# Kernel tuning notes

Measured on AMD Instinct MI355X. Metric: run time of the kernel, lower is better.

## Reference

```python
import jax, jax.numpy as jnp
import numpy as np

STRIDE = 8
OUT = 96                 # feature map size fh = fw
SEARCH = OUT * STRIDE    # 768, search image size
RATIOS = [0.33, 0.5, 1.0, 2.0, 3.0]
SCALES = [4, 8, 16]
PRE_NMS = 1024
POST_NMS = 256
NMS_THRESH = 0.7


def _make_anchors():
    # anchor widths/heights per (ratio, scale), base size = stride * scale
    ws, hs = [], []
    for r in RATIOS:
        for s in SCALES:
            ws.append(STRIDE * s / np.sqrt(r))
            hs.append(STRIDE * s * np.sqrt(r))
    ws = np.asarray(ws, np.float32)  # [A]
    hs = np.asarray(hs, np.float32)
    ori = SEARCH // 2 - (OUT // 2) * STRIDE
    c = ori + STRIDE * np.arange(OUT, dtype=np.float32)
    cy, cx = np.meshgrid(c, c, indexing="ij")  # [OUT, OUT]
    x1 = cx[None] - ws[:, None, None] * 0.5  # [A, OUT, OUT]
    y1 = cy[None] - hs[:, None, None] * 0.5
    x2 = cx[None] + ws[:, None, None] * 0.5
    y2 = cy[None] + hs[:, None, None] * 0.5
    return np.stack([x1, y1, x2, y2], axis=-1).reshape(-1, 4)  # [A*K, 4]


def setup_inputs() -> dict:
    key = jax.random.key(0)
    k1, k2 = jax.random.split(key)
    pred_cls = jax.random.normal(k1, (32, 30, 96, 96), jnp.float32)
    pred_reg = jax.random.normal(k2, (32, 60, 96, 96), jnp.float32) * 0.2
    anchors = jnp.asarray(_make_anchors())
    return {"pred_cls": pred_cls, "pred_reg": pred_reg, "anchors": anchors}


def _nms_pad(boxes, scores):
    """boxes [N,4] sorted by score desc, scores [N]. Returns [POST_NMS,5] padded."""
    x1, y1, x2, y2 = boxes[:, 0], boxes[:, 1], boxes[:, 2], boxes[:, 3]
    areas = (x2 - x1 + 1.0) * (y2 - y1 + 1.0)
    ix1 = jnp.maximum(x1[:, None], x1[None, :])
    iy1 = jnp.maximum(y1[:, None], y1[None, :])
    ix2 = jnp.minimum(x2[:, None], x2[None, :])
    iy2 = jnp.minimum(y2[:, None], y2[None, :])
    inter = jnp.maximum(ix2 - ix1 + 1.0, 0.0) * jnp.maximum(iy2 - iy1 + 1.0, 0.0)
    iou = inter / (areas[:, None] + areas[None, :] - inter)
    n = boxes.shape[0]
    idxs = jnp.arange(n)

    def body(keep, i):
        sup = keep[i] & (iou[i] > NMS_THRESH) & (idxs > i)
        return keep & ~sup, None

    keep, _ = jax.lax.scan(body, jnp.ones((n,), bool), idxs)
    pos = jnp.cumsum(keep) - 1
    dst = jnp.where(keep & (pos < POST_NMS), pos, POST_NMS)  # pad row for dropped
    rows = jnp.concatenate([scores[:, None], boxes], axis=1)  # [N,5] score first
    out = jnp.zeros((POST_NMS + 1, 5), boxes.dtype).at[dst].set(rows)
    return out[:POST_NMS]


def reference(pred_cls, pred_reg, anchors):
    b, a2, h, w = pred_cls.shape
    A = a2 // 2
    # log-softmax over the 2-way fg/bg channel; take foreground log-probs
    logp = jax.nn.log_softmax(pred_cls.reshape(b, 2, A, h, w), axis=1)
    scores = logp[:, 1].reshape(b, -1)  # [b, A*h*w]
    # deltas: (b,4A,h,w) -> (b,4,A,h,w) -> (b,A,h,w,4) -> (b,A*h*w,4)
    deltas = pred_reg.reshape(b, 4, A, h, w).transpose(0, 2, 3, 4, 1).reshape(b, -1, 4)
    aw = anchors[:, 2] - anchors[:, 0] + 1.0
    ah = anchors[:, 3] - anchors[:, 1] + 1.0
    acx = anchors[:, 0] + 0.5 * aw
    acy = anchors[:, 1] + 0.5 * ah
    dx, dy, dw, dh = deltas[..., 0], deltas[..., 1], deltas[..., 2], deltas[..., 3]
    pcx = dx * aw + acx
    pcy = dy * ah + acy
    pw = jnp.exp(dw) * aw
    ph = jnp.exp(dh) * ah
    boxes = jnp.stack([pcx - 0.5 * pw, pcy - 0.5 * ph, pcx + 0.5 * pw, pcy + 0.5 * ph], axis=-1)
    boxes = jnp.clip(boxes, 0.0, SEARCH - 1.0)  # clip to image
    top_s, top_i = jax.lax.top_k(scores, PRE_NMS)  # per-image pre-NMS top-k
    top_b = jnp.take_along_axis(boxes, top_i[..., None], axis=1)  # [b,PRE,4]
    return jax.vmap(_nms_pad)(top_b, top_s)  # [b, POST_NMS, 5]
```

## Files before the change

### kernel.cpp

```cpp
#include <hip/hip_runtime.h>
#include <stdint.h>

#define NANCH 138240
#define NANCH4 34560
#define B_CNT 32
#define PRE 1024
#define POST 256
#define BINS 8192
#define CAP 4096
#define SBLK 15
#define SLICE4 2304
#define TLOC 192
#define LOCCAP 273
#define PAD_KEY 0xFFFFFFFFFFFFFFFFull

typedef unsigned long long u64;

__device__ __forceinline__ unsigned key32(float sc) {
    unsigned u = __float_as_uint(sc);
    unsigned s = (u & 0x80000000u) ? ~u : (u | 0x80000000u);
    return ~s;
}

__device__ __forceinline__ unsigned key_of(float x0, float x1) {
    float m  = fmaxf(x0, x1);
    float e0 = expf(x0 - m);
    float e1 = expf(x1 - m);
    float sc = (x1 - m) - logf(e0 + e1);
    return key32(sc);
}

__device__ __forceinline__ void decode_box(const float* __restrict__ reg,
                                           const float* __restrict__ anch,
                                           int b, int idx, float box[4]) {
    const float* rb = reg + (size_t)b * 4 * NANCH;
    float dx = rb[idx];
    float dy = rb[idx + NANCH];
    float dw = rb[idx + 2 * NANCH];
    float dh = rb[idx + 3 * NANCH];
    float ax1 = anch[idx * 4 + 0], ay1 = anch[idx * 4 + 1];
    float ax2 = anch[idx * 4 + 2], ay2 = anch[idx * 4 + 3];
    float aw  = __fadd_rn(__fsub_rn(ax2, ax1), 1.0f);
    float ah  = __fadd_rn(__fsub_rn(ay2, ay1), 1.0f);
    float acx = __fadd_rn(ax1, __fmul_rn(0.5f, aw));
    float acy = __fadd_rn(ay1, __fmul_rn(0.5f, ah));
    float pcx = __fadd_rn(__fmul_rn(dx, aw), acx);
    float pcy = __fadd_rn(__fmul_rn(dy, ah), acy);
    float pw  = __fmul_rn(expf(dw), aw);
    float ph  = __fmul_rn(expf(dh), ah);
    float hx  = __fmul_rn(0.5f, pw);
    float hy  = __fmul_rn(0.5f, ph);
    box[0] = fminf(fmaxf(__fsub_rn(pcx, hx), 0.0f), 767.0f);
    box[1] = fminf(fmaxf(__fsub_rn(pcy, hy), 0.0f), 767.0f);
    box[2] = fminf(fmaxf(__fadd_rn(pcx, hx), 0.0f), 767.0f);
    box[3] = fminf(fmaxf(__fadd_rn(pcy, hy), 0.0f), 767.0f);
}

__global__ __launch_bounds__(1024) void select_kernel(const float* __restrict__ cls,
                                                      u64* __restrict__ cand) {
    __shared__ unsigned h[BINS];
    __shared__ unsigned s_wsum[16];
    __shared__ u64 loc[LOCCAP];
    __shared__ int s_b;
    __shared__ int lcnt;
    const int b = blockIdx.y;
    const int s = blockIdx.x;
    const int t = threadIdx.x;
    const int lane = t & 63, wid = t >> 6;
    if (t == 0) lcnt = 0;
    for (int i = t; i < BINS; i += 1024) h[i] = 0;
    __syncthreads();

    const float4* cb4 = (const float4*)(cls + (size_t)b * 2 * NANCH);
    const int base4 = s * SLICE4;

    for (int k = 0; k < 3; ++k) {
        int off = k * 1024 + t;
        if (off < SLICE4) {
            int g4 = base4 + off;
            float4 a0 = cb4[g4];
            float4 a1 = cb4[g4 + NANCH4];
            atomicAdd(&h[key_of(a0.x, a1.x) >> 19], 1u);
            atomicAdd(&h[key_of(a0.y, a1.y) >> 19], 1u);
            atomicAdd(&h[key_of(a0.z, a1.z) >> 19], 1u);
            atomicAdd(&h[key_of(a0.w, a1.w) >> 19], 1u);
        }
    }
    __syncthreads();

    unsigned bin[8];
    unsigned seg = 0;
    #pragma unroll
    for (int i = 0; i < 8; ++i) { bin[i] = h[t * 8 + i]; seg += bin[i]; }
    unsigned sc = seg;
    #pragma unroll
    for (int o = 1; o < 64; o <<= 1) {
        unsigned v = (unsigned)__shfl_up((int)sc, o);
        if (lane >= o) sc += v;
    }
    if (lane == 63) s_wsum[wid] = sc;
    __syncthreads();
    unsigned woff = 0;
    for (int i = 0; i < wid; ++i) woff += s_wsum[i];
    unsigned incl = sc + woff;
    unsigned excl = incl - seg;
    if (incl >= TLOC && excl < TLOC) {
        unsigned cum = excl;
        int bs = t * 8 + 7;
        for (int i = 0; i < 8; ++i) {
            if (cum + bin[i] >= TLOC) { bs = t * 8 + i; break; }
            cum += bin[i];
        }
        s_b = bs;
    }
    __syncthreads();
    const int bs = s_b;

    for (int k = 0; k < 3; ++k) {
        int off = k * 1024 + t;
        if (off < SLICE4) {
            int g4 = base4 + off;
            float4 a0 = cb4[g4];
            float4 a1 = cb4[g4 + NANCH4];
            float x0[4] = {a0.x, a0.y, a0.z, a0.w};
            float x1[4] = {a1.x, a1.y, a1.z, a1.w};
            #pragma unroll
            for (int j = 0; j < 4; ++j) {
                unsigned key = key_of(x0[j], x1[j]);
                if ((int)(key >> 19) <= bs) {
                    int pos = atomicAdd(&lcnt, 1);
                    if (pos < LOCCAP)
                        loc[pos] = ((u64)key << 32) | (unsigned)(g4 * 4 + j);
                }
            }
        }
    }
    __syncthreads();
    int n = lcnt; if (n > LOCCAP) n = LOCCAP;
    u64* segp = cand + (size_t)b * CAP + s * LOCCAP;
    for (int i = t; i < LOCCAP; i += 1024)
        segp[i] = (i < n) ? loc[i] : PAD_KEY;
    if (s == 0 && t == 0) cand[(size_t)b * CAP + (CAP - 1)] = PAD_KEY;
}

__global__ __launch_bounds__(512) void lsort_kernel(u64* __restrict__ cand) {
    __shared__ u64 sb[1024];
    const int c = blockIdx.x;
    const int b = blockIdx.y;
    const int t = threadIdx.x;
    u64* seg = cand + (size_t)b * CAP + c * 1024;
    for (int i = t; i < 1024; i += 512) sb[i] = seg[i];
    __syncthreads();
    for (int k = 2; k <= 1024; k <<= 1) {
        for (int j = k >> 1; j > 0; j >>= 1) {
            int i  = ((t & ~(j - 1)) << 1) | (t & (j - 1));
            int p  = i | j;
            bool up = ((i & k) == 0);
            u64 a = sb[i], bb = sb[p];
            if ((a > bb) == up) { sb[i] = bb; sb[p] = a; }
            __syncthreads();
        }
    }
    for (int i = t; i < 1024; i += 512) seg[i] = sb[i];
}

__global__ __launch_bounds__(1024) void merge_kernel(const u64* __restrict__ cand,
                                                     const float* __restrict__ reg,
                                                     const float* __restrict__ anch,
                                                     float* __restrict__ topS,
                                                     float* __restrict__ topB) {
    __shared__ u64 runs[CAP];
    const int r = blockIdx.x;
    const int b = blockIdx.y;
    const int t = threadIdx.x;
    for (int i = t; i < CAP; i += 1024) runs[i] = cand[(size_t)b * CAP + i];
    __syncthreads();

    u64 x = runs[r * 1024 + t];
    int rank = t;
    #pragma unroll
    for (int q = 0; q < 4; ++q) {
        if (q == r) continue;
        const u64* run = &runs[q * 1024];
        int lo = 0, hi = 1024;
        while (lo < hi) {
            int mid = (lo + hi) >> 1;
            if (run[mid] < x) lo = mid + 1; else hi = mid;
        }
        rank += lo;
    }
    if (rank < PRE) {
        int idx = (int)(x & 0xFFFFFFFFu);
        unsigned ks = (unsigned)(x >> 32);
        unsigned s  = ~ks;
        unsigned u  = (s & 0x80000000u) ? (s & 0x7FFFFFFFu) : ~s;
        float scv = __uint_as_float(u);
        float box[4];
        decode_box(reg, anch, b, idx, box);
        topS[b * PRE + rank] = scv;
        float* tb = topB + ((size_t)b * PRE + rank) * 4;
        tb[0] = box[0]; tb[1] = box[1]; tb[2] = box[2]; tb[3] = box[3];
    }
}

__global__ __launch_bounds__(1024) void mask_kernel(const float* __restrict__ topB,
                                                    u64* __restrict__ masks) {
    const int w = blockIdx.x;
    const int b = blockIdx.y;
    const int i = threadIdx.x;
    __shared__ float sx1[64], sy1[64], sx2[64], sy2[64], sar[64];
    if (i < 64) {
        const float* p = topB + ((size_t)b * PRE + w * 64 + i) * 4;
        float x1 = p[0], y1 = p[1], x2 = p[2], y2 = p[3];
        sx1[i] = x1; sy1[i] = y1; sx2[i] = x2; sy2[i] = y2;
        sar[i] = __fmul_rn(__fadd_rn(__fsub_rn(x2, x1), 1.0f),
                           __fadd_rn(__fsub_rn(y2, y1), 1.0f));
    }
    __syncthreads();
    const int jbase = w * 64;
    u64* dst = &masks[((size_t)b * PRE + i) * 16 + w];
    if (i >= jbase + 63) { *dst = 0ull; return; }
    const float* p = topB + ((size_t)b * PRE + i) * 4;
    float x1 = p[0], y1 = p[1], x2 = p[2], y2 = p[3];
    float ar = __fmul_rn(__fadd_rn(__fsub_rn(x2, x1), 1.0f),
                         __fadd_rn(__fsub_rn(y2, y1), 1.0f));
    u64 m = 0ull;
    for (int j = 0; j < 64; j++) {
        int jj = jbase + j;
        if (jj > i) {
            float ix1 = fmaxf(x1, sx1[j]);
            float iy1 = fmaxf(y1, sy1[j]);
            float ix2 = fminf(x2, sx2[j]);
            float iy2 = fminf(y2, sy2[j]);
            float iw = fmaxf(__fadd_rn(__fsub_rn(ix2, ix1), 1.0f), 0.0f);
            float ih = fmaxf(__fadd_rn(__fsub_rn(iy2, iy1), 1.0f), 0.0f);
            float inter = __fmul_rn(iw, ih);
            float denom = __fsub_rn(__fadd_rn(ar, sar[j]), inter);
            float iou = __fdiv_rn(inter, denom);
            if (iou > 0.7f) m |= (1ull << j);
        }
    }
    *dst = m;
}

__device__ __forceinline__ u64 shfl_xor_u64(u64 v, int lanemask) {
    int lo = __shfl_xor((int)(v & 0xFFFFFFFFull), lanemask);
    int hi = __shfl_xor((int)(v >> 32), lanemask);
    return ((u64)(unsigned)hi << 32) | (unsigned)lo;
}

__global__ __launch_bounds__(64) void nms_kernel(const u64* __restrict__ masks,
                                                 const float* __restrict__ topS,
                                                 const float* __restrict__ topB,
                                                 float* __restrict__ out) {
    const int b = blockIdx.x;
    const int t = threadIdx.x;
    __shared__ u64 rem[16];
    __shared__ int kept[POST];
    __shared__ int s_nk;
    if (t < 16) rem[t] = 0ull;
    __syncthreads();

    const u64* mb = masks + (size_t)b * PRE * 16;
    const int w = t >> 2, g = t & 3;
    int prefix = 0;

    u64 dv_cur = mb[(size_t)t * 16 + 0];
    u64 cw_cur[16];
    #pragma unroll
    for (int k = 0; k < 16; ++k)
        cw_cur[k] = mb[((size_t)(g * 16 + k)) * 16 + w];

    for (int c = 0; c < 16; ++c) {
        u64 dv_nxt = 0ull;
        u64 cw_nxt[16];
        if (c < 15) {
            const u64* nb = mb + (size_t)(c + 1) * 64 * 16;
            dv_nxt = nb[(size_t)t * 16 + (c + 1)];
            #pragma unroll
            for (int k = 0; k < 16; ++k)
                cw_nxt[k] = nb[((size_t)(g * 16 + k)) * 16 + w];
        } else {
            #pragma unroll
            for (int k = 0; k < 16; ++k) cw_nxt[k] = 0ull;
        }

        u64 alive = ~rem[c];
        int dlo = (int)(dv_cur & 0xFFFFFFFFull);
        int dhi = (int)(dv_cur >> 32);

        for (int l = 0; l < 64; ++l) {
            unsigned lo = (unsigned)__builtin_amdgcn_readlane(dlo, l);
            unsigned hi = (unsigned)__builtin_amdgcn_readlane(dhi, l);
            u64 dl = ((u64)hi << 32) | lo;
            u64 a = (alive >> l) & 1ull;
            alive &= ~(a ? dl : 0ull);
        }

        if ((alive >> t) & 1ull) {
            int pos = prefix + (int)__popcll(alive & ((1ull << t) - 1ull));
            if (pos < POST) kept[pos] = c * 64 + t;
        }
        prefix += (int)__popcll(alive);

        u64 acc = 0ull;
        #pragma unroll
        for (int k = 0; k < 16; ++k)
            if ((alive >> (g * 16 + k)) & 1ull) acc |= cw_cur[k];
        acc |= shfl_xor_u64(acc, 1);
        acc |= shfl_xor_u64(acc, 2);
        __syncthreads();
        if (g == 0 && w > c) rem[w] |= acc;
        __syncthreads();

        if (prefix >= POST) break;

        dv_cur = dv_nxt;
        #pragma unroll
        for (int k = 0; k < 16; ++k) cw_cur[k] = cw_nxt[k];
    }

    if (t == 0) s_nk = (prefix < POST) ? prefix : POST;
    __syncthreads();
    const int n = s_nk;

    float* ob = out + (size_t)b * POST * 5;
    for (int r = t; r < POST; r += 64) {
        if (r < n) {
            int i = kept[r];
            ob[r * 5 + 0] = topS[b * PRE + i];
            const float* tb = topB + ((size_t)b * PRE + i) * 4;
            ob[r * 5 + 1] = tb[0];
            ob[r * 5 + 2] = tb[1];
            ob[r * 5 + 3] = tb[2];
            ob[r * 5 + 4] = tb[3];
        } else {
            ob[r * 5 + 0] = 0.0f; ob[r * 5 + 1] = 0.0f; ob[r * 5 + 2] = 0.0f;
            ob[r * 5 + 3] = 0.0f; ob[r * 5 + 4] = 0.0f;
        }
    }
}

extern "C" void kernel_launch(void* const* d_in, const int* in_sizes, int n_in,
                              void* d_out, int out_size, void* d_ws, size_t ws_size,
                              hipStream_t stream) {
    const float* cls  = (const float*)d_in[0];
    const float* reg  = (const float*)d_in[1];
    const float* anch = (const float*)d_in[2];

    char* ws = (char*)d_ws;
    float* topS  = (float*)ws;
    float* topB  = (float*)(ws + 131072);
    u64*   cand  = (u64*)(ws + 655360);
    u64*   masks = (u64*)(ws + 1703936);

    select_kernel<<<dim3(SBLK, B_CNT), 1024, 0, stream>>>(cls, cand);
    lsort_kernel <<<dim3(4, B_CNT), 512, 0, stream>>>(cand);
    merge_kernel <<<dim3(4, B_CNT), 1024, 0, stream>>>(cand, reg, anch, topS, topB);
    mask_kernel  <<<dim3(16, B_CNT), 1024, 0, stream>>>(topB, masks);
    nms_kernel   <<<B_CNT, 64, 0, stream>>>(masks, topS, topB, (float*)d_out);
}
```

Measured before the change: 85.13 us.

## Sort candidates inside select kernel and merge 15 runs directly

Each select block now sorts its own candidate list in shared memory with a 512-element bitonic sort, which removes the separate lsort kernel launch. The merge kernel then ranks each candidate by binary-searching all 15 sorted runs of 273 entries instead of 4 runs of 1024. The scores computed in the histogram pass are also kept in registers, so the second pass no longer reloads cls from global memory or recomputes the log-softmax. The trade-offs are more binary searches per candidate, extra shared memory and barriers in select, and higher register pressure.

```diff
diff --git a/kernel.cpp b/kernel.cpp
--- a/kernel.cpp
+++ b/kernel.cpp
@@ -12,6 +12,7 @@
 #define SLICE4 2304
 #define TLOC 192
 #define LOCCAP 273
+#define SORTN 512
 #define PAD_KEY 0xFFFFFFFFFFFFFFFFull
 
 typedef unsigned long long u64;
@@ -59,8 +60,8 @@
 __global__ __launch_bounds__(1024) void select_kernel(const float* __restrict__ cls,
                                                       u64* __restrict__ cand) {
     __shared__ unsigned h[BINS];
+    __shared__ u64 sortbuf[SORTN];
     __shared__ unsigned s_wsum[16];
-    __shared__ u64 loc[LOCCAP];
     __shared__ int s_b;
     __shared__ int lcnt;
     const int b = blockIdx.y;
@@ -69,21 +70,28 @@
     const int lane = t & 63, wid = t >> 6;
     if (t == 0) lcnt = 0;
     for (int i = t; i < BINS; i += 1024) h[i] = 0;
+    if (t < SORTN) sortbuf[t] = PAD_KEY;
     __syncthreads();
 
     const float4* cb4 = (const float4*)(cls + (size_t)b * 2 * NANCH);
     const int base4 = s * SLICE4;
 
+    unsigned kk[3][4];
+    #pragma unroll
     for (int k = 0; k < 3; ++k) {
         int off = k * 1024 + t;
         if (off < SLICE4) {
             int g4 = base4 + off;
             float4 a0 = cb4[g4];
             float4 a1 = cb4[g4 + NANCH4];
-            atomicAdd(&h[key_of(a0.x, a1.x) >> 19], 1u);
-            atomicAdd(&h[key_of(a0.y, a1.y) >> 19], 1u);
-            atomicAdd(&h[key_of(a0.z, a1.z) >> 19], 1u);
-            atomicAdd(&h[key_of(a0.w, a1.w) >> 19], 1u);
+            kk[k][0] = key_of(a0.x, a1.x);
+            kk[k][1] = key_of(a0.y, a1.y);
+            kk[k][2] = key_of(a0.z, a1.z);
+            kk[k][3] = key_of(a0.w, a1.w);
+            atomicAdd(&h[kk[k][0] >> 19], 1u);
+            atomicAdd(&h[kk[k][1] >> 19], 1u);
+            atomicAdd(&h[kk[k][2] >> 19], 1u);
+            atomicAdd(&h[kk[k][3] >> 19], 1u);
         }
     }
     __syncthreads();
@@ -116,73 +124,62 @@
     __syncthreads();
     const int bs = s_b;
 
+    #pragma unroll
     for (int k = 0; k < 3; ++k) {
         int off = k * 1024 + t;
         if (off < SLICE4) {
             int g4 = base4 + off;
-            float4 a0 = cb4[g4];
-            float4 a1 = cb4[g4 + NANCH4];
-            float x0[4] = {a0.x, a0.y, a0.z, a0.w};
-            float x1[4] = {a1.x, a1.y, a1.z, a1.w};
             #pragma unroll
             for (int j = 0; j < 4; ++j) {
-                unsigned key = key_of(x0[j], x1[j]);
+                unsigned key = kk[k][j];
                 if ((int)(key >> 19) <= bs) {
                     int pos = atomicAdd(&lcnt, 1);
                     if (pos < LOCCAP)
-                        loc[pos] = ((u64)key << 32) | (unsigned)(g4 * 4 + j);
+                        sortbuf[pos] = ((u64)key << 32) | (unsigned)(g4 * 4 + j);
                 }
             }
         }
     }
     __syncthreads();
-    int n = lcnt; if (n > LOCCAP) n = LOCCAP;
+
+    for (int k = 2; k <= SORTN; k <<= 1) {
+        for (int j = k >> 1; j > 0; j >>= 1) {
+            if (t < SORTN / 2) {
+                int i = ((t & ~(j - 1)) << 1) | (t & (j - 1));
+                int p = i | j;
+                bool up = ((i & k) == 0);
+                u64 a = sortbuf[i], bb = sortbuf[p];
+                if ((a > bb) == up) { sortbuf[i] = bb; sortbuf[p] = a; }
+            }
+            __syncthreads();
+        }
+    }
+
     u64* segp = cand + (size_t)b * CAP + s * LOCCAP;
-    for (int i = t; i < LOCCAP; i += 1024)
-        segp[i] = (i < n) ? loc[i] : PAD_KEY;
+    for (int i = t; i < LOCCAP; i += 1024) segp[i] = sortbuf[i];
     if (s == 0 && t == 0) cand[(size_t)b * CAP + (CAP - 1)] = PAD_KEY;
 }
 
-__global__ __launch_bounds__(512) void lsort_kernel(u64* __restrict__ cand) {
-    __shared__ u64 sb[1024];
-    const int c = blockIdx.x;
+__global__ __launch_bounds__(512) void merge_kernel(const u64* __restrict__ cand,
+                                                    const float* __restrict__ reg,
+                                                    const float* __restrict__ anch,
+                                                    float* __restrict__ topS,
+                                                    float* __restrict__ topB) {
+    __shared__ u64 runs[CAP];
     const int b = blockIdx.y;
     const int t = threadIdx.x;
-    u64* seg = cand + (size_t)b * CAP + c * 1024;
-    for (int i = t; i < 1024; i += 512) sb[i] = seg[i];
-    __syncthreads();
-    for (int k = 2; k <= 1024; k <<= 1) {
-        for (int j = k >> 1; j > 0; j >>= 1) {
-            int i  = ((t & ~(j - 1)) << 1) | (t & (j - 1));
-            int p  = i | j;
-            bool up = ((i & k) == 0);
-            u64 a = sb[i], bb = sb[p];
-            if ((a > bb) == up) { sb[i] = bb; sb[p] = a; }
-            __syncthreads();
-        }
-    }
-    for (int i = t; i < 1024; i += 512) seg[i] = sb[i];
-}
-
-__global__ __launch_bounds__(1024) void merge_kernel(const u64* __restrict__ cand,
-                                                     const float* __restrict__ reg,
-                                                     const float* __restrict__ anch,
-                                                     float* __restrict__ topS,
-                                                     float* __restrict__ topB) {
-    __shared__ u64 runs[CAP];
-    const int r = blockIdx.x;
-    const int b = blockIdx.y;
-    const int t = threadIdx.x;
-    for (int i = t; i < CAP; i += 1024) runs[i] = cand[(size_t)b * CAP + i];
-    __syncthreads();
-
-    u64 x = runs[r * 1024 + t];
-    int rank = t;
-    #pragma unroll
-    for (int q = 0; q < 4; ++q) {
+    const int slot = blockIdx.x * 512 + t;
+    for (int i = t; i < CAP; i += 512) runs[i] = cand[(size_t)b * CAP + i];
+    __syncthreads();
+
+    u64 x = runs[slot];
+    if (x == PAD_KEY) return;
+    const int r = slot / LOCCAP;
+    int rank = slot - r * LOCCAP;
+    for (int q = 0; q < SBLK; ++q) {
         if (q == r) continue;
-        const u64* run = &runs[q * 1024];
-        int lo = 0, hi = 1024;
+        const u64* run = &runs[q * LOCCAP];
+        int lo = 0, hi = LOCCAP;
         while (lo < hi) {
             int mid = (lo + hi) >> 1;
             if (run[mid] < x) lo = mid + 1; else hi = mid;
@@ -355,8 +352,7 @@
     u64*   masks = (u64*)(ws + 1703936);
 
     select_kernel<<<dim3(SBLK, B_CNT), 1024, 0, stream>>>(cls, cand);
-    lsort_kernel <<<dim3(4, B_CNT), 512, 0, stream>>>(cand);
-    merge_kernel <<<dim3(4, B_CNT), 1024, 0, stream>>>(cand, reg, anch, topS, topB);
+    merge_kernel <<<dim3(8, B_CNT), 512, 0, stream>>>(cand, reg, anch, topS, topB);
     mask_kernel  <<<dim3(16, B_CNT), 1024, 0, stream>>>(topB, masks);
     nms_kernel   <<<B_CNT, 64, 0, stream>>>(masks, topS, topB, (float*)d_out);
 }
```

Measured after the change: 83.86 us, median of 2. Within noise of the previous version (-1.5%).
